# Kernel tuning notes

Measured on AMD Instinct MI355X. Metric: run time of the kernel, lower is better.

The kernel has to match this reference:

```python
import jax, jax.numpy as jnp
import numpy as np

# --- 5G LDPC BG1-structured code parameters (k=8000, n=16000, r=0.5) ---
Z = 384          # lifting factor
KB = 22          # info-bit base columns (BG1)
MB = 46          # base rows (BG1)
NB = 68          # base columns (BG1)
K = 8000         # info bits per codeword
N = 16000        # rate-matched codeword bits
BATCH = 2048
K_LDPC = KB * Z  # 8448
N_LDPC = NB * Z  # 26112
M_A = 4 * Z      # rows of A / size of B (core parity block)
M_C = (MB - 4) * Z  # 16128 remaining parity bits
NBPS = 4         # bits per QAM symbol (16-QAM interleaver)


def _lift(base_rows, base_cols, shifts):
    """Expand base-graph entries into lifted circulant (row, col) index lists."""
    br = np.asarray(base_rows, np.int64)
    bc = np.asarray(base_cols, np.int64)
    sh = np.asarray(shifts, np.int64)
    r = np.arange(Z, dtype=np.int64)
    rows = (br[:, None] * Z + r[None, :]).ravel()
    cols = (bc[:, None] * Z + (r[None, :] + sh[:, None]) % Z).ravel()
    order = np.argsort(rows, kind='stable')
    return rows[order].astype(np.int32), cols[order].astype(np.int32)


def _build_code_indices():
    rng = np.random.RandomState(0)
    mask = rng.rand(4, KB) < 0.35
    mask[:, 0] = True  # guarantee non-empty rows
    ar, ac = np.nonzero(mask)
    a_rows, a_cols = _lift(ar, ac, rng.randint(0, Z, size=ar.size))
    # B_inv: GF(2) inverse of lower-bidiagonal identity-block B ->
    # block lower-triangular of identity circulants (shift 0)
    br = [i for i in range(4) for j in range(i + 1)]
    bc = [j for i in range(4) for j in range(i + 1)]
    bi_rows, bi_cols = _lift(br, bc, np.zeros(len(br), np.int64))
    # C1: base rows 4..45 (local 0..41) x info cols 0..21
    mask = rng.rand(MB - 4, KB) < 0.15
    mask[:, 1] = True
    c1r, c1c = np.nonzero(mask)
    c1_rows, c1_cols = _lift(c1r, c1c, rng.randint(0, Z, size=c1r.size))
    # C2: base rows 4..45 (local) x core-parity cols 22..25 (local 0..3)
    mask = rng.rand(MB - 4, 4) < 0.35
    mask[:, 0] = True
    c2r, c2c = np.nonzero(mask)
    c2_rows, c2_cols = _lift(c2r, c2c, rng.randint(0, Z, size=c2r.size))
    # Output interleaver (Sec. 5.4.2.2): perm[i + j*m] = i*(n/m) + j
    out_int = np.arange(N, dtype=np.int32).reshape(NBPS, N // NBPS).T.ravel()
    return a_rows, a_cols, bi_rows, bi_cols, c1_rows, c1_cols, c2_rows, c2_cols, out_int


def setup_inputs() -> dict:
    key = jax.random.key(0)
    u = jax.random.randint(key, (BATCH, K), 0, 2).astype(jnp.float32)
    (a_rows, a_cols, bi_rows, bi_cols,
     c1_rows, c1_cols, c2_rows, c2_cols, out_int) = _build_code_indices()
    return {
        'u': u,
        'a_rows': jnp.asarray(a_rows), 'a_cols': jnp.asarray(a_cols),
        'bi_rows': jnp.asarray(bi_rows), 'bi_cols': jnp.asarray(bi_cols),
        'c1_rows': jnp.asarray(c1_rows), 'c1_cols': jnp.asarray(c1_cols),
        'c2_rows': jnp.asarray(c2_rows), 'c2_cols': jnp.asarray(c2_cols),
        'out_int': jnp.asarray(out_int),
    }


def _gf2_matmul(rows, cols, xT, m):
    """Sparse GF(2) matmul via gather + segment-sum + mod 2. xT: [dim_in, B]."""
    return jnp.mod(jax.ops.segment_sum(xT[cols], rows, num_segments=m), 2.0)


def reference(u, a_rows, a_cols, bi_rows, bi_cols,
              c1_rows, c1_cols, c2_rows, c2_cols, out_int):
    B = u.shape[0]
    # shortening: append k_ldpc - k filler zeros
    uT = jnp.concatenate([u, jnp.zeros((B, K_LDPC - K), u.dtype)], axis=1).T  # [k_ldpc, B]
    # core parity: p_a = B^-1 (A u)  over GF(2)
    auT = _gf2_matmul(a_rows, a_cols, uT, M_A)        # [4z, B]
    paT = _gf2_matmul(bi_rows, bi_cols, auT, M_A)     # [4z, B]
    # extension parity: p_b = C1 u + C2 p_a  over GF(2)
    s = (jax.ops.segment_sum(uT[c1_cols], c1_rows, num_segments=M_C)
         + jax.ops.segment_sum(paT[c2_cols], c2_rows, num_segments=M_C))
    pbT = jnp.mod(s, 2.0)                             # [42z, B]
    cT = jnp.concatenate([uT, paT, pbT], axis=0)      # [n_ldpc, B]
    # remove filler bits, puncture first 2z bits, take n bits
    c_nf = jnp.concatenate([cT[:K], cT[K_LDPC:]], axis=0)
    c_short = jax.lax.dynamic_slice_in_dim(c_nf, 2 * Z, N, axis=0)  # [n, B]
    # rate-matching output interleaver
    return c_short[out_int].T                          # [B, n]
```

## Files before the change

### kernel.cpp

```cpp
#include <hip/hip_runtime.h>
#include <stdint.h>

#define Zc      384
#define K_INFO  8000
#define N_OUT   16000
#define K_LDPC  8448
#define M_A     1536
#define PB_USED 7232
#define WPR     64
#define BATCH   2048

typedef float f4v __attribute__((ext_vector_type(4)));
typedef unsigned int u32;

#define OFF_UPACK 0
#define OFF_UT    2162688
#define OFF_PA    4325376
#define OFF_PAT   4718592
#define OFF_PBT   5111808
#define OFF_RPA   6963200
#define OFF_RPBI  6969600
#define OFF_RPC1  6976000
#define OFF_RPC2  7005184

__device__ __forceinline__ int lb(const int* __restrict__ a, int n, int key) {
  int lo = 0, hi = n;
  while (lo < hi) {
    int mid = (lo + hi) >> 1;
    if (a[mid] < key) lo = mid + 1; else hi = mid;
  }
  return lo;
}

__global__ __launch_bounds__(256) void k_rowptr(
    const int* __restrict__ a_rows, int na,
    const int* __restrict__ bi_rows, int nbi,
    const int* __restrict__ c1_rows, int nc1,
    const int* __restrict__ c2_rows, int nc2,
    int* __restrict__ rp_a, int* __restrict__ rp_bi,
    int* __restrict__ rp_c1, int* __restrict__ rp_c2) {
  const int i = blockIdx.x * 256 + threadIdx.x;
  if (i <= M_A)     { rp_a[i]  = lb(a_rows,  na,  i); rp_bi[i] = lb(bi_rows, nbi, i); }
  if (i <= PB_USED) { rp_c1[i] = lb(c1_rows, nc1, i); rp_c2[i] = lb(c2_rows, nc2, i); }
}

__global__ __launch_bounds__(256) void k_pack(const float* __restrict__ u,
                                              u32* __restrict__ u_pack,
                                              u32* __restrict__ uT) {
  __shared__ float tile[64][65];
  __shared__ uint64_t bw[64];
  const int k0 = blockIdx.x * 64;
  const int b0 = blockIdx.y * 64;
  const int tid = threadIdx.x;

  #pragma unroll
  for (int i = 0; i < 4; ++i) {
    int idx = tid + i * 256;
    int bb = idx >> 4, f4i = idx & 15;
    int k = k0 + f4i * 4;
    f4v v = (f4v)0.0f;
    if (k + 3 < K_INFO)
      v = __builtin_nontemporal_load(
            (const f4v*)(u + (size_t)(b0 + bb) * K_INFO + k));
    tile[bb][f4i*4+0] = v.x; tile[bb][f4i*4+1] = v.y;
    tile[bb][f4i*4+2] = v.z; tile[bb][f4i*4+3] = v.w;
  }
  __syncthreads();

  const int lane = tid & 63;
  const int wv   = tid >> 6;
  #pragma unroll
  for (int kk = 0; kk < 16; ++kk) {
    int kp = wv * 16 + kk;
    uint64_t m = __ballot(tile[lane][kp] != 0.0f);
    if (lane == 0) bw[kp] = m;
  }
  __syncthreads();

  if (tid < 64) {
    int row = k0 + tid;
    ((uint64_t*)(u_pack + (size_t)row * WPR))[blockIdx.y] = bw[tid];
  }
  if (tid < 128) {
    int half = tid >> 6, kk = tid & 63;
    uT[(size_t)(2 * blockIdx.y + half) * K_LDPC + k0 + kk] =
        (u32)(bw[kk] >> (32 * half));
  }
}

__global__ __launch_bounds__(256) void k_core(
    const int* __restrict__ a_cols,  const int* __restrict__ rp_a,
    const int* __restrict__ bi_cols, const int* __restrict__ rp_bi,
    const u32* __restrict__ u_pack,
    u32* __restrict__ pa, u32* __restrict__ paT) {
  const int r = blockIdx.x * 4 + (threadIdx.x >> 6);
  const int lane = threadIdx.x & 63;
  u32 acc = 0;
  const int lo = rp_bi[r], hi = rp_bi[r + 1];
  for (int e = lo; e < hi; ++e) {
    const int j = bi_cols[e];
    const int lo2 = rp_a[j], hi2 = rp_a[j + 1];
    for (int e2 = lo2; e2 < hi2; ++e2)
      acc ^= u_pack[(size_t)a_cols[e2] * WPR + lane];
  }
  pa[(size_t)r * WPR + lane] = acc;
  paT[(size_t)lane * M_A + r] = acc;
}

__global__ __launch_bounds__(256) void k_ext(
    const int* __restrict__ c1_cols, const int* __restrict__ rp_c1,
    const int* __restrict__ c2_cols, const int* __restrict__ rp_c2,
    const u32* __restrict__ u_pack, const u32* __restrict__ pa,
    u32* __restrict__ pbT) {
  const int r = blockIdx.x * 4 + (threadIdx.x >> 6);
  const int lane = threadIdx.x & 63;
  u32 acc = 0;
  int lo = rp_c1[r], hi = rp_c1[r + 1];
  for (int e = lo; e < hi; ++e)
    acc ^= u_pack[(size_t)c1_cols[e] * WPR + lane];
  lo = rp_c2[r]; hi = rp_c2[r + 1];
  for (int e = lo; e < hi; ++e)
    acc ^= pa[(size_t)c2_cols[e] * WPR + lane];
  pbT[(size_t)lane * PB_USED + r] = acc;
}

__global__ __launch_bounds__(256) void k_out(const u32* __restrict__ uT,
                                             const u32* __restrict__ paT,
                                             const u32* __restrict__ pbT,
                                             const int* __restrict__ out_int,
                                             float* __restrict__ out) {
  const int t = blockIdx.x * 256 + threadIdx.x;
  if (t >= N_OUT / 4) return;
  const int w = blockIdx.y;

  const int4 oi = *(const int4*)(out_int + 4 * t);
  const int rr[4] = {oi.x + 768, oi.y + 768, oi.z + 768, oi.w + 768};
  u32 wd[4];
  #pragma unroll
  for (int j = 0; j < 4; ++j) {
    const int row = rr[j];
    u32 v;
    if (row < 8000)      v = uT [(size_t)w * K_LDPC  + row];
    else if (row < 9536) v = paT[(size_t)w * M_A     + row - 8000];
    else                 v = pbT[(size_t)w * PB_USED + row - 9536];
    wd[j] = v;
  }

  float* op = out + (size_t)(w * 32) * N_OUT + 4 * t;
  #pragma unroll
  for (int bit = 0; bit < 32; ++bit) {
    f4v o;
    o.x = (float)((wd[0] >> bit) & 1u);
    o.y = (float)((wd[1] >> bit) & 1u);
    o.z = (float)((wd[2] >> bit) & 1u);
    o.w = (float)((wd[3] >> bit) & 1u);
    __builtin_nontemporal_store(o, (f4v*)(op + (size_t)bit * N_OUT));
  }
}

extern "C" void kernel_launch(void* const* d_in, const int* in_sizes, int n_in,
                              void* d_out, int out_size, void* d_ws, size_t ws_size,
                              hipStream_t stream) {
  const float* u      = (const float*)d_in[0];
  const int* a_rows   = (const int*)d_in[1];
  const int* a_cols   = (const int*)d_in[2];
  const int* bi_rows  = (const int*)d_in[3];
  const int* bi_cols  = (const int*)d_in[4];
  const int* c1_rows  = (const int*)d_in[5];
  const int* c1_cols  = (const int*)d_in[6];
  const int* c2_rows  = (const int*)d_in[7];
  const int* c2_cols  = (const int*)d_in[8];
  const int* out_int  = (const int*)d_in[9];
  const int na  = in_sizes[1];
  const int nbi = in_sizes[3];
  const int nc1 = in_sizes[5];
  const int nc2 = in_sizes[7];

  char* ws = (char*)d_ws;
  u32* u_pack = (u32*)(ws + OFF_UPACK);
  u32* uT     = (u32*)(ws + OFF_UT);
  u32* pa     = (u32*)(ws + OFF_PA);
  u32* paT    = (u32*)(ws + OFF_PAT);
  u32* pbT    = (u32*)(ws + OFF_PBT);
  int* rp_a   = (int*)(ws + OFF_RPA);
  int* rp_bi  = (int*)(ws + OFF_RPBI);
  int* rp_c1  = (int*)(ws + OFF_RPC1);
  int* rp_c2  = (int*)(ws + OFF_RPC2);
  float* out = (float*)d_out;

  k_rowptr<<<dim3((PB_USED + 256) / 256), 256, 0, stream>>>(
      a_rows, na, bi_rows, nbi, c1_rows, nc1, c2_rows, nc2,
      rp_a, rp_bi, rp_c1, rp_c2);
  k_pack<<<dim3(K_LDPC / 64, BATCH / 64), 256, 0, stream>>>(u, u_pack, uT);
  k_core<<<dim3(M_A / 4), 256, 0, stream>>>(a_cols, rp_a, bi_cols, rp_bi,
                                            u_pack, pa, paT);
  k_ext<<<dim3(PB_USED / 4), 256, 0, stream>>>(c1_cols, rp_c1, c2_cols, rp_c2,
                                               u_pack, pa, pbT);
  k_out<<<dim3((N_OUT / 4 + 255) / 256, WPR), 256, 0, stream>>>(uT, paT, pbT,
                                                                out_int, out);
}
```

Measured before the change: 235.6 us.

## Fuse row-pointer build into pack kernel and merge core/extension parity kernels

The row-pointer binary-search kernel now runs as extra blocks inside the pack kernel's grid. The core-parity and extension-parity kernels are merged into one launch, which removes the dependency on the intermediate pa buffer. Extension rows now recompute each needed core-parity word directly from u_pack through the B_inv and A sparse structures. This saves two launches and the serialisation between them, at the cost of redundant XOR gathers for the C2 terms. Whether that trade pays off depends on how heavy the launch overhead is compared with the extra gather work.

```diff
diff --git a/kernel.cpp b/kernel.cpp
--- a/kernel.cpp
+++ b/kernel.cpp
@@ -9,19 +9,20 @@
 #define PB_USED 7232
 #define WPR     64
 #define BATCH   2048
+#define PACK_TX 132
+#define RP_BX   29
 
 typedef float f4v __attribute__((ext_vector_type(4)));
 typedef unsigned int u32;
 
 #define OFF_UPACK 0
 #define OFF_UT    2162688
-#define OFF_PA    4325376
-#define OFF_PAT   4718592
-#define OFF_PBT   5111808
-#define OFF_RPA   6963200
-#define OFF_RPBI  6969600
-#define OFF_RPC1  6976000
-#define OFF_RPC2  7005184
+#define OFF_PAT   4325376
+#define OFF_PBT   4718592
+#define OFF_RPA   6569984
+#define OFF_RPBI  6576384
+#define OFF_RPC1  6582784
+#define OFF_RPC2  6611968
 
 __device__ __forceinline__ int lb(const int* __restrict__ a, int n, int key) {
   int lo = 0, hi = n;
@@ -32,26 +33,30 @@
   return lo;
 }
 
-__global__ __launch_bounds__(256) void k_rowptr(
-    const int* __restrict__ a_rows, int na,
-    const int* __restrict__ bi_rows, int nbi,
-    const int* __restrict__ c1_rows, int nc1,
-    const int* __restrict__ c2_rows, int nc2,
-    int* __restrict__ rp_a, int* __restrict__ rp_bi,
-    int* __restrict__ rp_c1, int* __restrict__ rp_c2) {
-  const int i = blockIdx.x * 256 + threadIdx.x;
-  if (i <= M_A)     { rp_a[i]  = lb(a_rows,  na,  i); rp_bi[i] = lb(bi_rows, nbi, i); }
-  if (i <= PB_USED) { rp_c1[i] = lb(c1_rows, nc1, i); rp_c2[i] = lb(c2_rows, nc2, i); }
-}
-
 __global__ __launch_bounds__(256) void k_pack(const float* __restrict__ u,
                                               u32* __restrict__ u_pack,
-                                              u32* __restrict__ uT) {
+                                              u32* __restrict__ uT,
+                                              const int* __restrict__ a_rows, int na,
+                                              const int* __restrict__ bi_rows, int nbi,
+                                              const int* __restrict__ c1_rows, int nc1,
+                                              const int* __restrict__ c2_rows, int nc2,
+                                              int* __restrict__ rp_a,
+                                              int* __restrict__ rp_bi,
+                                              int* __restrict__ rp_c1,
+                                              int* __restrict__ rp_c2) {
+  const int tid = threadIdx.x;
+  if (blockIdx.x >= PACK_TX) {
+    if (blockIdx.y != 0) return;
+    const int i = (blockIdx.x - PACK_TX) * 256 + tid;
+    if (i <= M_A)     { rp_a[i]  = lb(a_rows,  na,  i); rp_bi[i] = lb(bi_rows, nbi, i); }
+    if (i <= PB_USED) { rp_c1[i] = lb(c1_rows, nc1, i); rp_c2[i] = lb(c2_rows, nc2, i); }
+    return;
+  }
+
   __shared__ float tile[64][65];
   __shared__ uint64_t bw[64];
   const int k0 = blockIdx.x * 64;
   const int b0 = blockIdx.y * 64;
-  const int tid = threadIdx.x;
 
   #pragma unroll
   for (int i = 0; i < 4; ++i) {
@@ -88,40 +93,48 @@
   }
 }
 
-__global__ __launch_bounds__(256) void k_core(
+__global__ __launch_bounds__(256) void k_parity(
     const int* __restrict__ a_cols,  const int* __restrict__ rp_a,
     const int* __restrict__ bi_cols, const int* __restrict__ rp_bi,
-    const u32* __restrict__ u_pack,
-    u32* __restrict__ pa, u32* __restrict__ paT) {
-  const int r = blockIdx.x * 4 + (threadIdx.x >> 6);
-  const int lane = threadIdx.x & 63;
-  u32 acc = 0;
-  const int lo = rp_bi[r], hi = rp_bi[r + 1];
-  for (int e = lo; e < hi; ++e) {
-    const int j = bi_cols[e];
-    const int lo2 = rp_a[j], hi2 = rp_a[j + 1];
-    for (int e2 = lo2; e2 < hi2; ++e2)
-      acc ^= u_pack[(size_t)a_cols[e2] * WPR + lane];
-  }
-  pa[(size_t)r * WPR + lane] = acc;
-  paT[(size_t)lane * M_A + r] = acc;
-}
-
-__global__ __launch_bounds__(256) void k_ext(
     const int* __restrict__ c1_cols, const int* __restrict__ rp_c1,
     const int* __restrict__ c2_cols, const int* __restrict__ rp_c2,
-    const u32* __restrict__ u_pack, const u32* __restrict__ pa,
-    u32* __restrict__ pbT) {
-  const int r = blockIdx.x * 4 + (threadIdx.x >> 6);
+    const u32* __restrict__ u_pack,
+    u32* __restrict__ paT, u32* __restrict__ pbT) {
   const int lane = threadIdx.x & 63;
-  u32 acc = 0;
-  int lo = rp_c1[r], hi = rp_c1[r + 1];
-  for (int e = lo; e < hi; ++e)
-    acc ^= u_pack[(size_t)c1_cols[e] * WPR + lane];
-  lo = rp_c2[r]; hi = rp_c2[r + 1];
-  for (int e = lo; e < hi; ++e)
-    acc ^= pa[(size_t)c2_cols[e] * WPR + lane];
-  pbT[(size_t)lane * PB_USED + r] = acc;
+  const int wv   = threadIdx.x >> 6;
+  const int bx = blockIdx.x;
+
+  if (bx < M_A / 4) {
+    const int r = bx * 4 + wv;
+    u32 acc = 0;
+    const int lo = rp_bi[r], hi = rp_bi[r + 1];
+    for (int e = lo; e < hi; ++e) {
+      const int j = bi_cols[e];
+      const int lo2 = rp_a[j], hi2 = rp_a[j + 1];
+      for (int e2 = lo2; e2 < hi2; ++e2)
+        acc ^= u_pack[(size_t)a_cols[e2] * WPR + lane];
+    }
+    paT[(size_t)lane * M_A + r] = acc;
+  } else {
+    const int r = (bx - M_A / 4) * 4 + wv;
+    if (r >= PB_USED) return;
+    u32 acc = 0;
+    int lo = rp_c1[r], hi = rp_c1[r + 1];
+    for (int e = lo; e < hi; ++e)
+      acc ^= u_pack[(size_t)c1_cols[e] * WPR + lane];
+    lo = rp_c2[r]; hi = rp_c2[r + 1];
+    for (int e = lo; e < hi; ++e) {
+      const int p = c2_cols[e];
+      const int lo2 = rp_bi[p], hi2 = rp_bi[p + 1];
+      for (int e2 = lo2; e2 < hi2; ++e2) {
+        const int j = bi_cols[e2];
+        const int lo3 = rp_a[j], hi3 = rp_a[j + 1];
+        for (int e3 = lo3; e3 < hi3; ++e3)
+          acc ^= u_pack[(size_t)a_cols[e3] * WPR + lane];
+      }
+    }
+    pbT[(size_t)lane * PB_USED + r] = acc;
+  }
 }
 
 __global__ __launch_bounds__(256) void k_out(const u32* __restrict__ uT,
@@ -179,7 +192,6 @@
   char* ws = (char*)d_ws;
   u32* u_pack = (u32*)(ws + OFF_UPACK);
   u32* uT     = (u32*)(ws + OFF_UT);
-  u32* pa     = (u32*)(ws + OFF_PA);
   u32* paT    = (u32*)(ws + OFF_PAT);
   u32* pbT    = (u32*)(ws + OFF_PBT);
   int* rp_a   = (int*)(ws + OFF_RPA);
@@ -188,14 +200,12 @@
   int* rp_c2  = (int*)(ws + OFF_RPC2);
   float* out = (float*)d_out;
 
-  k_rowptr<<<dim3((PB_USED + 256) / 256), 256, 0, stream>>>(
-      a_rows, na, bi_rows, nbi, c1_rows, nc1, c2_rows, nc2,
+  k_pack<<<dim3(PACK_TX + RP_BX, BATCH / 64), 256, 0, stream>>>(
+      u, u_pack, uT, a_rows, na, bi_rows, nbi, c1_rows, nc1, c2_rows, nc2,
       rp_a, rp_bi, rp_c1, rp_c2);
-  k_pack<<<dim3(K_LDPC / 64, BATCH / 64), 256, 0, stream>>>(u, u_pack, uT);
-  k_core<<<dim3(M_A / 4), 256, 0, stream>>>(a_cols, rp_a, bi_cols, rp_bi,
-                                            u_pack, pa, paT);
-  k_ext<<<dim3(PB_USED / 4), 256, 0, stream>>>(c1_cols, rp_c1, c2_cols, rp_c2,
-                                               u_pack, pa, pbT);
+  k_parity<<<dim3(M_A / 4 + PB_USED / 4), 256, 0, stream>>>(
+      a_cols, rp_a, bi_cols, rp_bi, c1_cols, rp_c1, c2_cols, rp_c2,
+      u_pack, paT, pbT);
   k_out<<<dim3((N_OUT / 4 + 255) / 256, WPR), 256, 0, stream>>>(uT, paT, pbT,
                                                                 out_int, out);
 }
```

Result: no change. 232.8 us (-1.2%).
